# Performance work log

Measured on AMD Instinct MI355X. Metric: run time of the kernel, lower is better.

Reference implementation:

```python
import jax, jax.numpy as jnp
import numpy as np

B, L, D, H, E = 64, 128, 768, 2, 131072  # graphs, nodes/graph, hidden, heads, edges
N = B * L
C = D // H  # per-head channels


def _transformer_conv(x, src, dst, wq, bq, wk, bk, wv, bv, ws, bs):
    # PyG TransformerConv (concat=True, root_weight=True, beta=False)
    n = x.shape[0]
    q = (x @ wq + bq).reshape(n, H, C)
    k = (x @ wk + bk).reshape(n, H, C)
    v = (x @ wv + bv).reshape(n, H, C)
    # per-edge attention logits [E, H]
    logits = jnp.sum(q[dst] * k[src], axis=-1) * (1.0 / np.sqrt(C))
    # scatter softmax over incoming edges of each dst node
    m = jax.ops.segment_max(logits, dst, num_segments=n)
    e = jnp.exp(logits - m[dst])
    s = jax.ops.segment_sum(e, dst, num_segments=n)
    alpha = e / s[dst]  # [E, H]
    msg = alpha[..., None] * v[src]  # [E, H, C]
    agg = jax.ops.segment_sum(msg, dst, num_segments=n).reshape(n, D)
    return agg + x @ ws + bs


def setup_inputs() -> dict:
    key = jax.random.key(0)
    ks = jax.random.split(key, 24)
    x = jax.random.normal(ks[0], (N, D), jnp.float32)
    # within-graph random edges
    dst = jax.random.randint(ks[1], (E,), 0, N)
    off = jax.random.randint(ks[2], (E,), 0, L)
    src = (dst // L) * L + off
    edge_index = jnp.stack([src, dst]).astype(jnp.int32)

    def lin(k, i, o):
        return jax.random.normal(k, (i, o), jnp.float32) * 0.02

    inp = {"x": x, "edge_index": edge_index}
    i = 3
    for layer in ("1", "2"):
        for nm in ("wq", "wk", "wv", "ws"):
            inp[nm + layer] = lin(ks[i], D, D); i += 1
            inp["b" + nm[1] + layer] = jnp.zeros((D,), jnp.float32)
    inp["atti_w"] = lin(ks[i], 2 * D, D); i += 1
    inp["atti_b"] = jnp.zeros((D,), jnp.float32)
    inp["atts_w"] = lin(ks[i], D, 1); i += 1
    inp["atts_b"] = jnp.zeros((1,), jnp.float32)
    inp["fc1_w"] = lin(ks[i], D, D); i += 1
    inp["fc1_b"] = jnp.zeros((D,), jnp.float32)
    inp["fc2_w"] = lin(ks[i], D, 3); i += 1
    inp["fc2_b"] = jnp.zeros((3,), jnp.float32)
    return inp


def reference(x, edge_index, wq1, bq1, wk1, bk1, wv1, bv1, ws1, bs1,
              wq2, bq2, wk2, bk2, wv2, bv2, ws2, bs2,
              atti_w, atti_b, atts_w, atts_b, fc1_w, fc1_b, fc2_w, fc2_b):
    src, dst = edge_index[0], edge_index[1]
    h = jax.nn.relu(_transformer_conv(x, src, dst, wq1, bq1, wk1, bk1, wv1, bv1, ws1, bs1))
    h = jax.nn.relu(_transformer_conv(h, src, dst, wq2, bq2, wk2, bk2, wv2, bv2, ws2, bs2))
    # pad(): equal-size graphs -> reshape, mask all-valid (x_mask all False)
    hp = h.reshape(B, L, D)
    # attention pooling (eval path): query = first node of each graph
    x_q = jnp.broadcast_to(hp[:, :1], hp.shape)  # [B, L, D]
    x_c = jax.nn.relu(jnp.concatenate([x_q, hp], axis=-1) @ atti_w + atti_b)
    score = x_c @ atts_w + atts_b  # [B, L, 1]
    score = jax.nn.softmax(score, axis=1)
    pooled = jnp.sum(hp * score, axis=1)  # [B, D]
    out = jnp.tanh(pooled @ fc1_w + fc1_b) @ fc2_w + fc2_b
    return jax.nn.log_softmax(out, axis=-1)
```

## Files before the change

### kernel.cpp

```cpp
#include <hip/hip_runtime.h>

#define NN 8192
#define DD 768
#define EE 131072
#define BBg 64
#define LLn 128
#define CCh 384

typedef unsigned short u16;
typedef unsigned char u8;
typedef __attribute__((ext_vector_type(8))) short short8;
typedef __attribute__((ext_vector_type(4))) float f32x4;

__device__ __forceinline__ float b2f(u16 u) {
    union { unsigned int i; float f; } x; x.i = ((unsigned int)u) << 16; return x.f;
}
__device__ __forceinline__ u16 f2b(float f) {
    union { float f; unsigned int i; } x; x.f = f;
    unsigned int r = x.i + 0x7fffu + ((x.i >> 16) & 1u);
    return (u16)(r >> 16);
}
__device__ __forceinline__ void gload16(const void* g, void* l) {
    __builtin_amdgcn_global_load_lds((const __attribute__((address_space(1))) void*)g,
                                     (__attribute__((address_space(3))) void*)l, 16, 0, 0);
}

__global__ __launch_bounds__(256) void prep_kernel(const float* __restrict__ in,
                                                   u16* __restrict__ out,
                                                   unsigned int* __restrict__ cnt32,
                                                   float* __restrict__ score) {
    int i = blockIdx.x * 256 + threadIdx.x;
    float4 v = ((const float4*)in)[i];
    ushort4 o; o.x = f2b(v.x); o.y = f2b(v.y); o.z = f2b(v.z); o.w = f2b(v.w);
    ((ushort4*)out)[i] = o;
    if (blockIdx.x < 1024) cnt32[i] = 0;
    else if (blockIdx.x < 1056) score[i - 1024 * 256] = 0.f;
}

struct TP { const float* src; u16* dst; int rowOff; };
struct TP11 { TP a[11]; };

__global__ __launch_bounds__(256) void combo_kernel(TP11 args,
                                                    const int* __restrict__ srcp,
                                                    const int* __restrict__ dstp,
                                                    unsigned int* __restrict__ cnt32) {
    __shared__ float tile[64][65];
    if (blockIdx.z == 11) {
        for (int e = blockIdx.x * 256 + threadIdx.x; e < EE; e += 144 * 256) {
            int d = dstp[e], s = srcp[e];
            int g = d >> 7;
            int idx = (g << 14) + ((d & 127) << 7) + (s & 127);
            atomicAdd(&cnt32[idx >> 2], 1u << ((idx & 3) * 8));
        }
        return;
    }
    TP tp = args.a[blockIdx.z];
    int bx = blockIdx.x % 12, by = blockIdx.x / 12;
    int n0 = bx * 64, k0 = by * 64;
    int t = threadIdx.x;
    int tc = t & 63, tr = t >> 6;
#pragma unroll
    for (int i = 0; i < 16; i++)
        tile[tr + i * 4][tc] = tp.src[(size_t)(tp.rowOff + k0 + tr + i * 4) * DD + n0 + tc];
    __syncthreads();
#pragma unroll
    for (int i = 0; i < 16; i++) {
        int row = tr + i * 4;
        tp.dst[(size_t)(n0 + row) * DD + k0 + tc] = f2b(tile[tc][row]);
    }
}

enum { EPI_F32 = 1, EPI_TANH = 3 };

__global__ __launch_bounds__(256) void gemm_bf16(const u16* __restrict__ A,
                                                 const u16* __restrict__ Wt,
                                                 const float* __restrict__ bias,
                                                 void* __restrict__ outp, int K, int mode) {
    __shared__ u16 As[64][72];
    __shared__ u16 Bs[64][72];
    const int m0 = blockIdx.y * 64, n0 = blockIdx.x * 64;
    const int t = threadIdx.x;
    const int lane = t & 63, w = t >> 6;
    const int tr = t >> 2, tc = (t & 3) * 16;
    f32x4 acc[4] = {{0,0,0,0},{0,0,0,0},{0,0,0,0},{0,0,0,0}};
    const int fRow = lane & 15;
    const int fK = (lane >> 4) * 8;

    for (int k0 = 0; k0 < K; k0 += 64) {
        int4 a0 = *(const int4*)(A + (size_t)(m0 + tr) * K + k0 + tc);
        int4 a1 = *(const int4*)(A + (size_t)(m0 + tr) * K + k0 + tc + 8);
        int4 b0 = *(const int4*)(Wt + (size_t)(n0 + tr) * K + k0 + tc);
        int4 b1 = *(const int4*)(Wt + (size_t)(n0 + tr) * K + k0 + tc + 8);
        __syncthreads();
        *(int4*)&As[tr][tc] = a0; *(int4*)&As[tr][tc + 8] = a1;
        *(int4*)&Bs[tr][tc] = b0; *(int4*)&Bs[tr][tc + 8] = b1;
        __syncthreads();
#pragma unroll
        for (int s = 0; s < 2; s++) {
            short8 af = *(const short8*)&As[w * 16 + fRow][s * 32 + fK];
#pragma unroll
            for (int g = 0; g < 4; g++) {
                short8 bf = *(const short8*)&Bs[g * 16 + fRow][s * 32 + fK];
                acc[g] = __builtin_amdgcn_mfma_f32_16x16x32_bf16(af, bf, acc[g], 0, 0, 0);
            }
        }
    }
    const int colLocal = lane & 15;
    const int rowLocal = (lane >> 4) * 4;
#pragma unroll
    for (int g = 0; g < 4; g++) {
        int col = n0 + g * 16 + colLocal;
        float bv = bias ? bias[col] : 0.f;
#pragma unroll
        for (int i = 0; i < 4; i++) {
            int row = m0 + w * 16 + rowLocal + i;
            float v = acc[g][i] + bv;
            if (mode == EPI_TANH) v = tanhf(v);
            ((float*)outp)[(size_t)row * DD + col] = v;
        }
    }
}

#define SLAB 24576
__global__ __launch_bounds__(512, 2) void gemm256(const u16* __restrict__ A,
                                                  const u16* __restrict__ Wt,
                                                  const float* __restrict__ b0,
                                                  const float* __restrict__ b1,
                                                  const float* __restrict__ b2,
                                                  const float* __restrict__ b3,
                                                  u16* __restrict__ o0, u16* __restrict__ o1,
                                                  u16* __restrict__ o2, u16* __restrict__ o3) {
    __shared__ u16 smem[3 * SLAB];
    const int K = DD;
    const int t = threadIdx.x;
    const int lane = t & 63, w = t >> 6;
    const int wr = w >> 1, wc = w & 1;
    const int m0 = blockIdx.y * 256, n0 = blockIdx.x * 128;
    const int fRow = lane & 15, fThr = lane >> 4;
    const u16* Abase = A + (size_t)m0 * K;
    const u16* Bbase = Wt + (size_t)n0 * K;

    auto stage = [&](u16* slab, int kt2, int j) {
        const int k0 = kt2 * 64;
        if (j < 4) {
            int c = t + 512 * j;
            int row = c >> 3;
            int col = ((c & 7) ^ (row & 7)) * 8;
            gload16(Abase + (size_t)row * K + k0 + col, (char*)slab + (size_t)c * 16);
        } else {
            int c = t + 512 * (j - 4);
            int row = c >> 3;
            int col = ((c & 7) ^ (row & 7)) * 8;
            gload16(Bbase + (size_t)row * K + k0 + col, (char*)(slab + 16384) + (size_t)c * 16);
        }
    };

#pragma unroll
    for (int j = 0; j < 6; ++j) stage(smem, 0, j);
#pragma unroll
    for (int j = 0; j < 6; ++j) stage(smem + SLAB, 1, j);
    asm volatile("s_waitcnt vmcnt(6)" ::: "memory");
    __builtin_amdgcn_s_barrier();

    f32x4 acc[4][4] = {};
    int cur = 0;
    for (int kt = 0; kt < 12; ++kt) {
        const u16* As = smem + cur * SLAB;
        const u16* Bs = As + 16384;
        int nx = cur + 2; if (nx >= 3) nx -= 3;
        u16* slabN = smem + nx * SLAB;
        const bool pf = (kt < 10);

        short8 af[4][2];
#pragma unroll
        for (int kk2 = 0; kk2 < 2; ++kk2) {
            const int cj = kk2 * 4 + fThr;
#pragma unroll
            for (int i = 0; i < 4; ++i) {
                const int R = wr * 64 + i * 16 + fRow;
                af[i][kk2] = *(const short8*)&As[((size_t)R * 8 + (cj ^ (R & 7))) * 8];
            }
        }
        short8 bfA[2][2];
#pragma unroll
        for (int kk2 = 0; kk2 < 2; ++kk2) {
            const int cj = kk2 * 4 + fThr;
#pragma unroll
            for (int g = 0; g < 2; ++g) {
                const int Rb = wc * 64 + g * 16 + fRow;
                bfA[g][kk2] = *(const short8*)&Bs[((size_t)Rb * 8 + (cj ^ (Rb & 7))) * 8];
            }
        }
        if (pf) { stage(slabN, kt + 2, 0); stage(slabN, kt + 2, 1); stage(slabN, kt + 2, 2); }
        __builtin_amdgcn_s_barrier();
        asm volatile("s_waitcnt lgkmcnt(0)" ::: "memory");
        __builtin_amdgcn_s_setprio(1);
#pragma unroll
        for (int kk2 = 0; kk2 < 2; ++kk2)
#pragma unroll
            for (int i = 0; i < 4; ++i)
#pragma unroll
                for (int g = 0; g < 2; ++g)
                    acc[i][g] = __builtin_amdgcn_mfma_f32_16x16x32_bf16(af[i][kk2], bfA[g][kk2],
                                                                        acc[i][g], 0, 0, 0);
        __builtin_amdgcn_s_setprio(0);
        __builtin_amdgcn_s_barrier();
        short8 bfB[2][2];
#pragma unroll
        for (int kk2 = 0; kk2 < 2; ++kk2) {
            const int cj = kk2 * 4 + fThr;
#pragma unroll
            for (int g = 0; g < 2; ++g) {
                const int Rb = wc * 64 + (g + 2) * 16 + fRow;
                bfB[g][kk2] = *(const short8*)&Bs[((size_t)Rb * 8 + (cj ^ (Rb & 7))) * 8];
            }
        }
        if (pf) { stage(slabN, kt + 2, 3); stage(slabN, kt + 2, 4); stage(slabN, kt + 2, 5); }
        __builtin_amdgcn_s_barrier();
        asm volatile("s_waitcnt lgkmcnt(0)" ::: "memory");
        __builtin_amdgcn_s_setprio(1);
#pragma unroll
        for (int kk2 = 0; kk2 < 2; ++kk2)
#pragma unroll
            for (int i = 0; i < 4; ++i)
#pragma unroll
                for (int g = 0; g < 2; ++g)
                    acc[i][g + 2] = __builtin_amdgcn_mfma_f32_16x16x32_bf16(af[i][kk2], bfB[g][kk2],
                                                                            acc[i][g + 2], 0, 0, 0);
        __builtin_amdgcn_s_setprio(0);
        if (kt < 10) asm volatile("s_waitcnt vmcnt(6)" ::: "memory");
        else if (kt == 10) asm volatile("s_waitcnt vmcnt(0)" ::: "memory");
        __builtin_amdgcn_s_barrier();
        cur += 1; if (cur == 3) cur = 0;
    }

    const int chunk = n0 / DD;
    const float* bp = (chunk == 0) ? b0 : (chunk == 1) ? b1 : (chunk == 2) ? b2 : b3;
    u16* op = (chunk == 0) ? o0 : (chunk == 1) ? o1 : (chunk == 2) ? o2 : o3;
    const int cb0 = n0 - chunk * DD;
    if (chunk == 2) {
        u16 (*Vt)[264] = (u16(*)[264])smem;
#pragma unroll
        for (int g = 0; g < 4; g++) {
            float bv = bp[cb0 + wc * 64 + g * 16 + fRow];
#pragma unroll
            for (int i = 0; i < 4; i++)
#pragma unroll
                for (int rr = 0; rr < 4; rr++)
                    Vt[wc * 64 + g * 16 + fRow][wr * 64 + i * 16 + fThr * 4 + rr] =
                        f2b(acc[i][g][rr] + bv);
        }
        __syncthreads();
#pragma unroll
        for (int ii = 0; ii < 16; ii++) {
            int c = t + 512 * ii;
            int col = c >> 6, ch = c & 63;
            *(ushort4*)(op + (size_t)(cb0 + col) * NN + m0 + ch * 4) =
                *(const ushort4*)&Vt[col][ch * 4];
        }
    } else {
        u16 (*Cs)[136] = (u16(*)[136])smem;
#pragma unroll
        for (int g = 0; g < 4; g++) {
            float bv = bp[cb0 + wc * 64 + g * 16 + fRow];
#pragma unroll
            for (int i = 0; i < 4; i++)
#pragma unroll
                for (int rr = 0; rr < 4; rr++)
                    Cs[wr * 64 + i * 16 + fThr * 4 + rr][wc * 64 + g * 16 + fRow] =
                        f2b(acc[i][g][rr] + bv);
        }
        __syncthreads();
#pragma unroll
        for (int ii = 0; ii < 16; ii++) {
            int c = t + 512 * ii;
            int row = c >> 5, ch = c & 31;
            *(ushort4*)(op + (size_t)(m0 + row) * DD + cb0 + ch * 4) =
                *(const ushort4*)&Cs[row][ch * 4];
        }
    }
}

__global__ __launch_bounds__(256) void gemm_xc(const u16* __restrict__ A,
                                               const u16* __restrict__ Wt,
                                               const u16* __restrict__ wt8,
                                               const float* __restrict__ atti_b,
                                               const float* __restrict__ atts_w,
                                               float* __restrict__ score) {
    __shared__ u16 As[128 * 64];
    __shared__ u16 Bs[128 * 64];
    __shared__ float aq_p[2][128];
    const int K = DD;
    const int t = threadIdx.x;
    const int lane = t & 63, w = t >> 6;
    const int wr = w >> 1, wc = w & 1;
    const int n0 = blockIdx.x * 128, m0 = blockIdx.y * 128;
    const int fRow = lane & 15, fThr = lane >> 4;

    {
        int col = t & 127, kh = t >> 7;
        const u16* xr = A + (size_t)m0 * DD + kh * 384;
        const u16* wr8 = wt8 + (size_t)(n0 + col) * DD + kh * 384;
        float s = 0.f;
#pragma unroll 8
        for (int j = 0; j < 96; j++) {
            ushort4 a4 = *(const ushort4*)(xr + j * 4);
            ushort4 b4 = *(const ushort4*)(wr8 + j * 4);
            s += b2f(a4.x) * b2f(b4.x) + b2f(a4.y) * b2f(b4.y)
               + b2f(a4.z) * b2f(b4.z) + b2f(a4.w) * b2f(b4.w);
        }
        aq_p[kh][col] = s;
    }

    f32x4 acc[4][4] = {};
    const u16* Abase = A + (size_t)m0 * K;
    const u16* Bbase = Wt + (size_t)n0 * K;
    for (int k0 = 0; k0 < K; k0 += 64) {
        __syncthreads();
#pragma unroll
        for (int i = 0; i < 4; i++) {
            int c = t + 256 * i;
            int row = c >> 3;
            int col = ((c & 7) ^ (row & 7)) * 8;
            gload16(Abase + (size_t)row * K + k0 + col, (char*)As + (size_t)c * 16);
            gload16(Bbase + (size_t)row * K + k0 + col, (char*)Bs + (size_t)c * 16);
        }
        __syncthreads();
#pragma unroll
        for (int kk = 0; kk < 64; kk += 32) {
            const int cjW = (kk >> 3) + fThr;
            short8 af[4], bf[4];
#pragma unroll
            for (int i = 0; i < 4; i++) {
                int R = wr * 64 + i * 16 + fRow;
                af[i] = *(const short8*)&As[(R * 8 + (cjW ^ (R & 7))) * 8];
            }
#pragma unroll
            for (int g = 0; g < 4; g++) {
                int R = wc * 64 + g * 16 + fRow;
                bf[g] = *(const short8*)&Bs[(R * 8 + (cjW ^ (R & 7))) * 8];
            }
#pragma unroll
            for (int i = 0; i < 4; i++)
#pragma unroll
                for (int g = 0; g < 4; g++)
                    acc[i][g] = __builtin_amdgcn_mfma_f32_16x16x32_bf16(af[i], bf[g], acc[i][g], 0, 0, 0);
        }
    }
    float rsum[4][4] = {};
#pragma unroll
    for (int g = 0; g < 4; g++) {
        int cl = wc * 64 + g * 16 + fRow;
        int col = n0 + cl;
        float bv = atti_b[col] + aq_p[0][cl] + aq_p[1][cl];
        float av = atts_w[col];
#pragma unroll
        for (int i = 0; i < 4; i++)
#pragma unroll
            for (int rr = 0; rr < 4; rr++) {
                float v = fmaxf(acc[i][g][rr] + bv, 0.f);
                rsum[i][rr] += v * av;
            }
    }
#pragma unroll
    for (int i = 0; i < 4; i++)
#pragma unroll
        for (int rr = 0; rr < 4; rr++) {
            float s = rsum[i][rr];
            s += __shfl_xor(s, 1, 16); s += __shfl_xor(s, 2, 16);
            s += __shfl_xor(s, 4, 16); s += __shfl_xor(s, 8, 16);
            if (fRow == 0)
                atomicAdd(&score[m0 + wr * 64 + i * 16 + fThr * 4 + rr], s);
        }
}

__global__ __launch_bounds__(256) void attn_fused(const u16* __restrict__ qb,
                                                  const u16* __restrict__ kb,
                                                  const u16* __restrict__ vT,
                                                  const u8* __restrict__ cnt,
                                                  const u16* __restrict__ hs,
                                                  u16* __restrict__ out) {
    __shared__ u16 As[64][72];
    __shared__ u16 Bs[128][72];
    __shared__ u16 Pl[64][136];
    __shared__ u16 Vt[64][136];
    const int half = blockIdx.x, hd = blockIdx.y, g = blockIdx.z;
    const int t = threadIdx.x;
    const int lane = t & 63, w = t >> 6;
    const int fRow = lane & 15, fThr = lane >> 4;
    const int dstBase = g * 128 + half * 64;
    const u16* Qb = qb + (size_t)dstBase * DD + hd * CCh;
    const u16* Kb = kb + (size_t)(g * 128) * DD + hd * CCh;

    f32x4 acc[8] = {};
    const int trA = t >> 2, tcA = (t & 3) * 16;
    const int trB = t >> 1, tcB = (t & 1) * 32;
    for (int k0 = 0; k0 < CCh; k0 += 64) {
        int4 a0 = *(const int4*)(Qb + (size_t)trA * DD + k0 + tcA);
        int4 a1 = *(const int4*)(Qb + (size_t)trA * DD + k0 + tcA + 8);
        int4 b0 = *(const int4*)(Kb + (size_t)trB * DD + k0 + tcB);
        int4 b1 = *(const int4*)(Kb + (size_t)trB * DD + k0 + tcB + 8);
        int4 b2 = *(const int4*)(Kb + (size_t)trB * DD + k0 + tcB + 16);
        int4 b3 = *(const int4*)(Kb + (size_t)trB * DD + k0 + tcB + 24);
        __syncthreads();
        *(int4*)&As[trA][tcA] = a0; *(int4*)&As[trA][tcA + 8] = a1;
        *(int4*)&Bs[trB][tcB] = b0; *(int4*)&Bs[trB][tcB + 8] = b1;
        *(int4*)&Bs[trB][tcB + 16] = b2; *(int4*)&Bs[trB][tcB + 24] = b3;
        __syncthreads();
#pragma unroll
        for (int kk = 0; kk < 64; kk += 32) {
            short8 af = *(const short8*)&As[w * 16 + fRow][kk + fThr * 8];
#pragma unroll
            for (int j = 0; j < 8; j++) {
                short8 bf = *(const short8*)&Bs[j * 16 + fRow][kk + fThr * 8];
                acc[j] = __builtin_amdgcn_mfma_f32_16x16x32_bf16(af, bf, acc[j], 0, 0, 0);
            }
        }
    }

    const float scale = 0.05103103630798288f;
    const u8* cg = cnt + ((size_t)g << 14);
    const int rbase = half * 64 + w * 16 + fThr * 4;
    float pv[8][4];
#pragma unroll
    for (int i = 0; i < 4; i++) {
        float m = -3.4e38f;
#pragma unroll
        for (int j = 0; j < 8; j++) {
            float c = (float)cg[(rbase + i) * 128 + j * 16 + fRow];
            float s = acc[j][i] * scale;
            pv[j][i] = c;
            if (c > 0.f) m = fmaxf(m, s);
        }
#pragma unroll
        for (int msk = 1; msk <= 8; msk <<= 1) m = fmaxf(m, __shfl_xor(m, msk, 16));
        float sum = 0.f;
#pragma unroll
        for (int j = 0; j < 8; j++) {
            float p = (pv[j][i] > 0.f) ? pv[j][i] * __expf(acc[j][i] * scale - m) : 0.f;
            pv[j][i] = p; sum += p;
        }
#pragma unroll
        for (int msk = 1; msk <= 8; msk <<= 1) sum += __shfl_xor(sum, msk, 16);
        float inv = (sum > 0.f) ? 1.f / sum : 0.f;
#pragma unroll
        for (int j = 0; j < 8; j++)
            Pl[w * 16 + fThr * 4 + i][j * 16 + fRow] = f2b(pv[j][i] * inv);
    }

    for (int cc = 0; cc < 6; cc++) {
        __syncthreads();
#pragma unroll
        for (int ii = 0; ii < 4; ii++) {
            int q = t + 256 * ii;
            int row = q >> 4, col = (q & 15) * 8;
            *(int4*)&Vt[row][col] =
                *(const int4*)(vT + (size_t)(hd * CCh + cc * 64 + row) * NN + g * 128 + col);
        }
        __syncthreads();
        f32x4 acc2[4] = {};
#pragma unroll
        for (int kk = 0; kk < 128; kk += 32) {
            short8 af = *(const short8*)&Pl[w * 16 + fRow][kk + fThr * 8];
#pragma unroll
            for (int j = 0; j < 4; j++) {
                short8 bf = *(const short8*)&Vt[j * 16 + fRow][kk + fThr * 8];
                acc2[j] = __builtin_amdgcn_mfma_f32_16x16x32_bf16(af, bf, acc2[j], 0, 0, 0);
            }
        }
#pragma unroll
        for (int j = 0; j < 4; j++) {
            int c = hd * CCh + cc * 64 + j * 16 + fRow;
#pragma unroll
            for (int i = 0; i < 4; i++) {
                int row = dstBase + w * 16 + fThr * 4 + i;
                size_t idx = (size_t)row * DD + c;
                float r = fmaxf(acc2[j][i] + b2f(hs[idx]), 0.f);
                out[idx] = f2b(r);
            }
        }
    }
}

__global__ __launch_bounds__(192) void pool_kernel(const float* __restrict__ score,
                                                   const u16* __restrict__ hx,
                                                   u16* __restrict__ pb) {
    int b = blockIdx.x, t = threadIdx.x;
    __shared__ float sprob[LLn];
    if (t < 64) {
        float s0 = score[b * LLn + t];
        float s1 = score[b * LLn + 64 + t];
        float mx = fmaxf(s0, s1);
#pragma unroll
        for (int m = 1; m <= 32; m <<= 1) mx = fmaxf(mx, __shfl_xor(mx, m, 64));
        float e0 = __expf(s0 - mx), e1 = __expf(s1 - mx);
        float sum = e0 + e1;
#pragma unroll
        for (int m = 1; m <= 32; m <<= 1) sum += __shfl_xor(sum, m, 64);
        float inv = 1.f / sum;
        sprob[t] = e0 * inv; sprob[t + 64] = e1 * inv;
    }
    __syncthreads();
    int c = t * 4;
    float a0 = 0, a1 = 0, a2 = 0, a3 = 0;
    for (int l = 0; l < LLn; l++) {
        float wl = sprob[l];
        ushort4 hv = *(const ushort4*)(hx + (size_t)(b * LLn + l) * DD + c);
        a0 += wl * b2f(hv.x); a1 += wl * b2f(hv.y); a2 += wl * b2f(hv.z); a3 += wl * b2f(hv.w);
    }
    ushort4 o; o.x = f2b(a0); o.y = f2b(a1); o.z = f2b(a2); o.w = f2b(a3);
    *(ushort4*)(pb + (size_t)b * DD + c) = o;
}

__global__ __launch_bounds__(256) void head2_kernel(const float* __restrict__ u,
                                                    const float* __restrict__ fc2w,
                                                    const float* __restrict__ fc2b,
                                                    float* __restrict__ outp) {
    int b = blockIdx.x, t = threadIdx.x;
    __shared__ float sred[4][3];
    float p0 = 0, p1 = 0, p2 = 0;
    for (int k = t; k < DD; k += 256) {
        float uv = u[(size_t)b * DD + k];
        p0 += uv * fc2w[k * 3 + 0]; p1 += uv * fc2w[k * 3 + 1]; p2 += uv * fc2w[k * 3 + 2];
    }
#pragma unroll
    for (int m = 1; m <= 32; m <<= 1) {
        p0 += __shfl_xor(p0, m, 64); p1 += __shfl_xor(p1, m, 64); p2 += __shfl_xor(p2, m, 64);
    }
    int w = t >> 6, lane = t & 63;
    if (lane == 0) { sred[w][0] = p0; sred[w][1] = p1; sred[w][2] = p2; }
    __syncthreads();
    if (t == 0) {
        float z0 = fc2b[0], z1 = fc2b[1], z2 = fc2b[2];
        for (int i = 0; i < 4; i++) { z0 += sred[i][0]; z1 += sred[i][1]; z2 += sred[i][2]; }
        float mx = fmaxf(z0, fmaxf(z1, z2));
        float lse = mx + logf(__expf(z0 - mx) + __expf(z1 - mx) + __expf(z2 - mx));
        outp[b * 3 + 0] = z0 - lse; outp[b * 3 + 1] = z1 - lse; outp[b * 3 + 2] = z2 - lse;
    }
}

static inline char* carve(char*& p, size_t bytes) {
    char* r = p;
    p += (bytes + 255) & ~(size_t)255;
    return r;
}

extern "C" void kernel_launch(void* const* d_in, const int* in_sizes, int n_in,
                              void* d_out, int out_size, void* d_ws, size_t ws_size,
                              hipStream_t stream) {
    const float* x = (const float*)d_in[0];
    const int* ei = (const int*)d_in[1];
    const int* srcp = ei;
    const int* dstp = ei + EE;
    const float* wL[8] = {(const float*)d_in[2], (const float*)d_in[4], (const float*)d_in[6],
                          (const float*)d_in[8], (const float*)d_in[10], (const float*)d_in[12],
                          (const float*)d_in[14], (const float*)d_in[16]};
    const float* bL[8] = {(const float*)d_in[3], (const float*)d_in[5], (const float*)d_in[7],
                          (const float*)d_in[9], (const float*)d_in[11], (const float*)d_in[13],
                          (const float*)d_in[15], (const float*)d_in[17]};
    const float* atti_w = (const float*)d_in[18];
    const float* atti_b = (const float*)d_in[19];
    const float* atts_w = (const float*)d_in[20];
    const float* fc1_w = (const float*)d_in[22];
    const float* fc1_b = (const float*)d_in[23];
    const float* fc2_w = (const float*)d_in[24];
    const float* fc2_b = (const float*)d_in[25];
    float* outp = (float*)d_out;

    char* p = (char*)d_ws;
    const size_t ndb = (size_t)NN * DD * 2;
    const size_t wsz = (size_t)DD * DD * 2;
    u16* qb = (u16*)carve(p, ndb);
    u16* kb = (u16*)carve(p, ndb);
    u16* vt = (u16*)carve(p, ndb);
    u16* xb = (u16*)carve(p, ndb);
    u16* hb = (u16*)carve(p, ndb);
    u16* hs = (u16*)carve(p, ndb);
    u16* wtcat1 = (u16*)carve(p, wsz * 4);
    u16* wtcat2 = (u16*)carve(p, wsz * 4);
    u16* wt8 = (u16*)carve(p, wsz);
    u16* wt9 = (u16*)carve(p, wsz);
    u16* wtfc1 = (u16*)carve(p, wsz);
    u16* pb = (u16*)carve(p, (size_t)BBg * DD * 2);
    float* uu = (float*)carve(p, (size_t)BBg * DD * 4);
    u8* cnt = (u8*)carve(p, (size_t)BBg * 128 * 128);
    float* score = (float*)carve(p, NN * 4);

    prep_kernel<<<6144, 256, 0, stream>>>(x, xb, (unsigned int*)cnt, score);

    TP11 tps;
    for (int i = 0; i < 4; i++) tps.a[i] = {wL[i], wtcat1 + (size_t)i * DD * DD, 0};
    for (int i = 0; i < 4; i++) tps.a[4 + i] = {wL[4 + i], wtcat2 + (size_t)i * DD * DD, 0};
    tps.a[8] = {atti_w, wt8, 0};
    tps.a[9] = {atti_w, wt9, DD};
    tps.a[10] = {fc1_w, wtfc1, 0};
    combo_kernel<<<dim3(144, 1, 12), 256, 0, stream>>>(tps, srcp, dstp, (unsigned int*)cnt);

    dim3 gf(24, 32);
    dim3 ga(2, 2, BBg);
    gemm256<<<gf, 512, 0, stream>>>(xb, wtcat1, bL[0], bL[1], bL[2], bL[3], qb, kb, vt, hs);
    attn_fused<<<ga, 256, 0, stream>>>(qb, kb, vt, cnt, hs, hb);
    gemm256<<<gf, 512, 0, stream>>>(hb, wtcat2, bL[4], bL[5], bL[6], bL[7], qb, kb, vt, hs);
    attn_fused<<<ga, 256, 0, stream>>>(qb, kb, vt, cnt, hs, xb);

    gemm_xc<<<dim3(6, 64), 256, 0, stream>>>(xb, wt9, wt8, atti_b, atts_w, score);

    pool_kernel<<<BBg, 192, 0, stream>>>(score, xb, pb);
    gemm_bf16<<<dim3(12, 1), 256, 0, stream>>>(pb, wtfc1, fc1_b, uu, DD, EPI_TANH);
    head2_kernel<<<BBg, 256, 0, stream>>>(uu, fc2_w, fc2_b, outp);
}
```

Measured before the change: 329.6 us.

## Restructure GEMM main loop into k-half ping-pong with XCD-aware block remap

The GEMM main loop now splits each 64-wide k tile into two halves. Fragments for the next half are loaded from LDS while MFMAs run on the current half, with partial lgkmcnt waits and sched barriers replacing the full waits and extra barriers. Global prefetch of the whole next-next slab is issued at the top of each iteration. Block IDs are also remapped so that neighbouring tiles land on the same XCD, which is meant to improve L2 reuse of A and W. This holds more fragment registers live, which adds register pressure at 2 blocks per CU.

```diff
diff --git a/kernel.cpp b/kernel.cpp
--- a/kernel.cpp
+++ b/kernel.cpp
@@ -135,32 +135,53 @@
     const int t = threadIdx.x;
     const int lane = t & 63, w = t >> 6;
     const int wr = w >> 1, wc = w & 1;
-    const int m0 = blockIdx.y * 256, n0 = blockIdx.x * 128;
+    const int id = blockIdx.y * 24 + blockIdx.x;
+    const int xcd = id & 7, jj = id >> 3;
+    const int by = (xcd >> 1) * 8 + jj / 12;
+    const int bx = (xcd & 1) * 12 + jj % 12;
+    const int m0 = by * 256, n0 = bx * 128;
     const int fRow = lane & 15, fThr = lane >> 4;
     const u16* Abase = A + (size_t)m0 * K;
     const u16* Bbase = Wt + (size_t)n0 * K;
 
-    auto stage = [&](u16* slab, int kt2, int j) {
+    auto stage = [&](u16* slab, int kt2) {
         const int k0 = kt2 * 64;
-        if (j < 4) {
-            int c = t + 512 * j;
+#pragma unroll
+        for (int s = 0; s < 4; ++s) {
+            int c = t + 512 * s;
             int row = c >> 3;
             int col = ((c & 7) ^ (row & 7)) * 8;
             gload16(Abase + (size_t)row * K + k0 + col, (char*)slab + (size_t)c * 16);
-        } else {
-            int c = t + 512 * (j - 4);
+        }
+#pragma unroll
+        for (int s = 0; s < 2; ++s) {
+            int c = t + 512 * s;
             int row = c >> 3;
             int col = ((c & 7) ^ (row & 7)) * 8;
             gload16(Bbase + (size_t)row * K + k0 + col, (char*)(slab + 16384) + (size_t)c * 16);
         }
     };
-
-#pragma unroll
-    for (int j = 0; j < 6; ++j) stage(smem, 0, j);
-#pragma unroll
-    for (int j = 0; j < 6; ++j) stage(smem + SLAB, 1, j);
+    auto loadFrags = [&](const u16* As, const u16* Bs, int p, short8* af, short8* bf) {
+        const int cj = p * 4 + fThr;
+#pragma unroll
+        for (int i = 0; i < 4; ++i) {
+            const int R = wr * 64 + i * 16 + fRow;
+            af[i] = *(const short8*)&As[((size_t)R * 8 + (cj ^ (R & 7))) * 8];
+        }
+#pragma unroll
+        for (int g = 0; g < 4; ++g) {
+            const int Rb = wc * 64 + g * 16 + fRow;
+            bf[g] = *(const short8*)&Bs[((size_t)Rb * 8 + (cj ^ (Rb & 7))) * 8];
+        }
+    };
+
+    stage(smem, 0);
+    stage(smem + SLAB, 1);
     asm volatile("s_waitcnt vmcnt(6)" ::: "memory");
     __builtin_amdgcn_s_barrier();
+
+    short8 afA[4], bfA[4], afB[4], bfB[4];
+    loadFrags(smem, smem + 16384, 0, afA, bfA);
 
     f32x4 acc[4][4] = {};
     int cur = 0;
@@ -168,70 +189,41 @@
         const u16* As = smem + cur * SLAB;
         const u16* Bs = As + 16384;
         int nx = cur + 2; if (nx >= 3) nx -= 3;
-        u16* slabN = smem + nx * SLAB;
-        const bool pf = (kt < 10);
-
-        short8 af[4][2];
-#pragma unroll
-        for (int kk2 = 0; kk2 < 2; ++kk2) {
-            const int cj = kk2 * 4 + fThr;
-#pragma unroll
-            for (int i = 0; i < 4; ++i) {
-                const int R = wr * 64 + i * 16 + fRow;
-                af[i][kk2] = *(const short8*)&As[((size_t)R * 8 + (cj ^ (R & 7))) * 8];
-            }
-        }
-        short8 bfA[2][2];
-#pragma unroll
-        for (int kk2 = 0; kk2 < 2; ++kk2) {
-            const int cj = kk2 * 4 + fThr;
-#pragma unroll
-            for (int g = 0; g < 2; ++g) {
-                const int Rb = wc * 64 + g * 16 + fRow;
-                bfA[g][kk2] = *(const short8*)&Bs[((size_t)Rb * 8 + (cj ^ (Rb & 7))) * 8];
-            }
-        }
-        if (pf) { stage(slabN, kt + 2, 0); stage(slabN, kt + 2, 1); stage(slabN, kt + 2, 2); }
+        int pv = cur + 1; if (pv >= 3) pv -= 3;
+        if (kt < 10) stage(smem + nx * SLAB, kt + 2);
+
+        loadFrags(As, Bs, 1, afB, bfB);
+        asm volatile("s_waitcnt lgkmcnt(8)" ::: "memory");
+        __builtin_amdgcn_sched_barrier(0);
+        __builtin_amdgcn_s_setprio(1);
+#pragma unroll
+        for (int i = 0; i < 4; ++i)
+#pragma unroll
+            for (int g = 0; g < 4; ++g)
+                acc[i][g] = __builtin_amdgcn_mfma_f32_16x16x32_bf16(afA[i], bfA[g], acc[i][g], 0, 0, 0);
+        __builtin_amdgcn_s_setprio(0);
+
+        if (kt < 10) asm volatile("s_waitcnt vmcnt(6)" ::: "memory");
+        else         asm volatile("s_waitcnt vmcnt(0)" ::: "memory");
         __builtin_amdgcn_s_barrier();
-        asm volatile("s_waitcnt lgkmcnt(0)" ::: "memory");
+
+        if (kt < 11) {
+            loadFrags(smem + pv * SLAB, smem + pv * SLAB + 16384, 0, afA, bfA);
+            asm volatile("s_waitcnt lgkmcnt(8)" ::: "memory");
+        } else {
+            asm volatile("s_waitcnt lgkmcnt(0)" ::: "memory");
+        }
+        __builtin_amdgcn_sched_barrier(0);
         __builtin_amdgcn_s_setprio(1);
 #pragma unroll
-        for (int kk2 = 0; kk2 < 2; ++kk2)
-#pragma unroll
-            for (int i = 0; i < 4; ++i)
-#pragma unroll
-                for (int g = 0; g < 2; ++g)
-                    acc[i][g] = __builtin_amdgcn_mfma_f32_16x16x32_bf16(af[i][kk2], bfA[g][kk2],
-                                                                        acc[i][g], 0, 0, 0);
+        for (int i = 0; i < 4; ++i)
+#pragma unroll
+            for (int g = 0; g < 4; ++g)
+                acc[i][g] = __builtin_amdgcn_mfma_f32_16x16x32_bf16(afB[i], bfB[g], acc[i][g], 0, 0, 0);
         __builtin_amdgcn_s_setprio(0);
         __builtin_amdgcn_s_barrier();
-        short8 bfB[2][2];
-#pragma unroll
-        for (int kk2 = 0; kk2 < 2; ++kk2) {
-            const int cj = kk2 * 4 + fThr;
-#pragma unroll
-            for (int g = 0; g < 2; ++g) {
-                const int Rb = wc * 64 + (g + 2) * 16 + fRow;
-                bfB[g][kk2] = *(const short8*)&Bs[((size_t)Rb * 8 + (cj ^ (Rb & 7))) * 8];
-            }
-        }
-        if (pf) { stage(slabN, kt + 2, 3); stage(slabN, kt + 2, 4); stage(slabN, kt + 2, 5); }
-        __builtin_amdgcn_s_barrier();
-        asm volatile("s_waitcnt lgkmcnt(0)" ::: "memory");
-        __builtin_amdgcn_s_setprio(1);
-#pragma unroll
-        for (int kk2 = 0; kk2 < 2; ++kk2)
-#pragma unroll
-            for (int i = 0; i < 4; ++i)
-#pragma unroll
-                for (int g = 0; g < 2; ++g)
-                    acc[i][g + 2] = __builtin_amdgcn_mfma_f32_16x16x32_bf16(af[i][kk2], bfB[g][kk2],
-                                                                            acc[i][g + 2], 0, 0, 0);
-        __builtin_amdgcn_s_setprio(0);
-        if (kt < 10) asm volatile("s_waitcnt vmcnt(6)" ::: "memory");
-        else if (kt == 10) asm volatile("s_waitcnt vmcnt(0)" ::: "memory");
-        __builtin_amdgcn_s_barrier();
-        cur += 1; if (cur == 3) cur = 0;
+
+        cur = pv;
     }
 
     const int chunk = n0 / DD;
```

New measurement: 343.2 us. 4.1% more time.
